# Performance work log

Hardware: AMD Instinct MI355X
Metric: run time of the kernel (lower is better)

The kernel has to match this reference:

```python
import jax, jax.numpy as jnp
import numpy as np

N = 50000
E = 800000
IN_C = 128
HID = 32
HEADS = 8
OUT_C = 64
NEG_SLOPE = 0.2


def setup_inputs() -> dict:
    key = jax.random.key(0)
    ks = jax.random.split(key, 12)
    x = jax.random.normal(ks[0], (N, IN_C), dtype=jnp.float32)
    edge_index = jax.random.randint(ks[1], (2, E), 0, N, dtype=jnp.int64)
    s = 0.05
    W1 = jax.random.normal(ks[2], (IN_C, HEADS * HID), dtype=jnp.float32) * s
    a1_src = jax.random.normal(ks[3], (HEADS, HID), dtype=jnp.float32) * s
    a1_dst = jax.random.normal(ks[4], (HEADS, HID), dtype=jnp.float32) * s
    b1 = jnp.zeros((HEADS * HID,), dtype=jnp.float32)
    W2 = jax.random.normal(ks[5], (HEADS * HID, OUT_C), dtype=jnp.float32) * s
    a2_src = jax.random.normal(ks[6], (1, OUT_C), dtype=jnp.float32) * s
    a2_dst = jax.random.normal(ks[7], (1, OUT_C), dtype=jnp.float32) * s
    b2 = jnp.zeros((OUT_C,), dtype=jnp.float32)
    return {"x": x, "edge_index": edge_index, "W1": W1, "a1_src": a1_src,
            "a1_dst": a1_dst, "b1": b1, "W2": W2, "a2_src": a2_src,
            "a2_dst": a2_dst, "b2": b2}


def gat_conv(x, W, a_src, a_dst, bias, src, dst, concat):
    # x: [N, F_in]; W: [F_in, H*C]; a_src/a_dst: [H, C]
    H, C = a_src.shape
    h = (x @ W).reshape(N, H, C)                      # [N, H, C]
    alpha_s = jnp.einsum('nhc,hc->nh', h, a_src)      # [N, H]
    alpha_d = jnp.einsum('nhc,hc->nh', h, a_dst)
    e = alpha_s[src] + alpha_d[dst]                   # [E, H]
    e = jnp.where(e >= 0, e, NEG_SLOPE * e)           # leaky relu
    # segment softmax over destination nodes
    m = jax.ops.segment_max(e, dst, num_segments=N)   # [N, H]
    e = jnp.exp(e - m[dst])
    z = jax.ops.segment_sum(e, dst, num_segments=N)   # [N, H]
    alpha = e / z[dst]                                # [E, H]
    msg = h[src] * alpha[:, :, None]                  # [E, H, C]
    out = jax.ops.segment_sum(msg, dst, num_segments=N)  # [N, H, C]
    if concat:
        out = out.reshape(N, H * C)
    else:
        out = out.mean(axis=1)
    return out + bias


def reference(x, edge_index, W1, a1_src, a1_dst, b1, W2, a2_src, a2_dst, b2):
    src, dst = edge_index[0], edge_index[1]
    # dropout omitted (eval mode)
    h = gat_conv(x, W1, a1_src, a1_dst, b1, src, dst, concat=True)
    h = jax.nn.elu(h)
    out = gat_conv(h, W2, a2_src, a2_dst, b2, src, dst, concat=False)
    return out
```

## Files before the change

kernel.cpp:

```cpp
#include <hip/hip_runtime.h>
#include <cstdint>
#include <cstddef>

#define N_NODES 50000
#define N_EDGES 800000
#define INC 128
#define HID 32
#define HEADS 8
#define OUTC 64
#define F1 (HEADS * HID)
#define NEG 0.2f
#define CAP 64

typedef unsigned short bf16_t;
typedef __attribute__((ext_vector_type(8))) short bf16x8;
typedef __attribute__((ext_vector_type(4))) float f32x4;

__device__ __forceinline__ float bf2f(bf16_t u) {
  union { unsigned int i; float f; } v;
  v.i = ((unsigned int)u) << 16;
  return v.f;
}
__device__ __forceinline__ bf16_t f2bf(float x) {
  union { float f; unsigned int u; } v;
  v.f = x;
  unsigned int r = v.u + 0x7FFFu + ((v.u >> 16) & 1u);
  return (bf16_t)(r >> 16);
}
__device__ __forceinline__ float lrexp(float v) {
  return expf((v >= 0.f) ? v : NEG * v);
}

__global__ __launch_bounds__(256) void prep(
    const float* __restrict__ W1, const float* __restrict__ W2,
    bf16_t* __restrict__ W1T, bf16_t* __restrict__ W2T, int* __restrict__ cnt) {
  int t = blockIdx.x * 256 + threadIdx.x;
  if (t < N_NODES) cnt[t] = 0;
  if (t < INC * F1) {
    int k = t >> 8, n = t & 255;
    W1T[(size_t)n * INC + k] = f2bf(W1[t]);
  }
  if (t < F1 * OUTC) {
    int k = t >> 6, n = t & 63;
    W2T[(size_t)n * F1 + k] = f2bf(W2[t]);
  }
}

template <bool AF32, int HPT, int HTOT>
__global__ __launch_bounds__(256) void mfma_gemm_fused(
    const void* __restrict__ Av, const bf16_t* __restrict__ Wt,
    bf16_t* __restrict__ C, const float* __restrict__ a_src,
    const float* __restrict__ a_dst, float* __restrict__ as,
    float* __restrict__ ad, int M, int N, int K,
    const int* __restrict__ srcE, const int* __restrict__ dstE,
    int* __restrict__ cnt, int* __restrict__ bucket) {
  constexpr int BM = 64, BN = 64, BK = 64;
  __shared__ union SM {
    bf16_t A[BM * BK];
    struct { float ct[64][65]; float pr[64][4]; } epi;
  } sm;

  const int tid = threadIdx.x;

  if (cnt != nullptr) {
    int eid = (blockIdx.y * gridDim.x + blockIdx.x) * 256 + tid;
    if (eid < N_EDGES) {
      int dd = dstE[eid];
      int pos = atomicAdd(&cnt[dd], 1);
      bucket[(size_t)dd * CAP + pos] = srcE[eid];
    }
  }

  const int wave = tid >> 6, lane = tid & 63;
  const int wm = (wave >> 1) * 32, wn = (wave & 1) * 32;
  const int lr = lane & 15, lq = lane >> 4;
  const int m0 = blockIdx.y * BM, n0 = blockIdx.x * BN;
  const float* A32 = (const float*)Av;
  const bf16_t* A16 = (const bf16_t*)Av;

  f32x4 acc[2][2] = {};

  for (int k0 = 0; k0 < K; k0 += BK) {
    bf16x8 bcur[2][2];
#pragma unroll
    for (int ni = 0; ni < 2; ni++) {
      const size_t brow = (size_t)(n0 + wn + ni * 16 + lr) * K;
#pragma unroll
      for (int kk = 0; kk < 2; kk++)
        bcur[kk][ni] = *reinterpret_cast<const bf16x8*>(
            &Wt[brow + k0 + kk * 32 + lq * 8]);
    }

#pragma unroll
    for (int p = 0; p < 2; p++) {
      int id = p * 256 + tid;
      int r = id >> 3, c = id & 7;
      int gm = m0 + r;
      uint4 v = make_uint4(0, 0, 0, 0);
      if constexpr (AF32) {
        if (gm < M) {
          const float4* ap =
              reinterpret_cast<const float4*>(&A32[(size_t)gm * K + k0 + c * 8]);
          float4 v0 = ap[0], v1 = ap[1];
          union { bf16_t h[8]; uint4 u; } pk;
          pk.h[0] = f2bf(v0.x); pk.h[1] = f2bf(v0.y);
          pk.h[2] = f2bf(v0.z); pk.h[3] = f2bf(v0.w);
          pk.h[4] = f2bf(v1.x); pk.h[5] = f2bf(v1.y);
          pk.h[6] = f2bf(v1.z); pk.h[7] = f2bf(v1.w);
          v = pk.u;
        }
      } else {
        if (gm < M) v = *reinterpret_cast<const uint4*>(&A16[(size_t)gm * K + k0 + c * 8]);
      }
      *reinterpret_cast<uint4*>(&sm.A[r * BK + ((c ^ (r & 7)) * 8)]) = v;
    }
    __syncthreads();
#pragma unroll
    for (int kk = 0; kk < 2; kk++) {
      bf16x8 af[2];
#pragma unroll
      for (int mi = 0; mi < 2; mi++) {
        int rr = wm + mi * 16 + lr;
        af[mi] = *reinterpret_cast<const bf16x8*>(
            &sm.A[rr * BK + (((kk * 4 + lq) ^ (rr & 7)) * 8)]);
      }
#pragma unroll
      for (int mi = 0; mi < 2; mi++)
#pragma unroll
        for (int ni = 0; ni < 2; ni++)
          acc[mi][ni] = __builtin_amdgcn_mfma_f32_16x16x32_bf16(
              af[mi], bcur[kk][ni], acc[mi][ni], 0, 0, 0);
    }
    __syncthreads();
  }

#pragma unroll
  for (int mi = 0; mi < 2; mi++)
#pragma unroll
    for (int ni = 0; ni < 2; ni++)
#pragma unroll
      for (int r = 0; r < 4; r++)
        sm.epi.ct[wm + mi * 16 + lq * 4 + r][wn + ni * 16 + lr] = acc[mi][ni][r];
  __syncthreads();

  {
    int row = tid >> 2, ch = tid & 3;
    int gm = m0 + row;
    if (gm < M) {
      union { bf16_t h[8]; uint4 u; } pk0, pk1;
#pragma unroll
      for (int c = 0; c < 8; c++) pk0.h[c] = f2bf(sm.epi.ct[row][ch * 16 + c]);
#pragma unroll
      for (int c = 0; c < 8; c++) pk1.h[c] = f2bf(sm.epi.ct[row][ch * 16 + 8 + c]);
      *reinterpret_cast<uint4*>(&C[(size_t)gm * N + n0 + ch * 16]) = pk0.u;
      *reinterpret_cast<uint4*>(&C[(size_t)gm * N + n0 + ch * 16 + 8]) = pk1.u;
    }
  }

  {
    int row = tid >> 2, part = tid & 3;
    int gn = m0 + row;
    const float* av = ((part & 2) ? a_dst : a_src) + n0 + (part & 1) * 32;
    float dot = 0.f;
#pragma unroll
    for (int c = 0; c < 32; c++) dot += sm.epi.ct[row][(part & 1) * 32 + c] * av[c];
    if constexpr (HPT == 2) {
      if (gn < M) {
        float* tgt = (part & 2) ? ad : as;
        tgt[(size_t)gn * HTOT + (n0 >> 5) + (part & 1)] = dot;
      }
    } else {
      sm.epi.pr[row][part] = dot;
      __syncthreads();
      if (part == 0 && gn < M) {
        as[gn] = sm.epi.pr[row][0] + sm.epi.pr[row][1];
        ad[gn] = sm.epi.pr[row][2] + sm.epi.pr[row][3];
      }
    }
  }
}

__global__ __launch_bounds__(256) void gat_aggr1(
    const int* __restrict__ cnt, const int* __restrict__ bucket,
    const float* __restrict__ as, const float* __restrict__ ad,
    const bf16_t* __restrict__ hb, const float* __restrict__ bias,
    bf16_t* __restrict__ outp) {
  int d = blockIdx.x * 4 + (threadIdx.x >> 6);
  int lane = threadIdx.x & 63;
  if (d >= N_NODES) return;
  int deg = cnt[d];
  const int* bkt = bucket + (size_t)d * CAP;
  const int sh = lane & 7;
  const int es = lane >> 3;
  const int ah = lane >> 3;
  float ad_h = ad[(size_t)d * 8 + sh];
  float a0 = 0.f, a1 = 0.f, a2 = 0.f, a3 = 0.f, zacc = 0.f;

  if (deg > 0) {
    int ei = es;
    int s_reg = bkt[(ei < deg) ? ei : deg - 1];
    float w_reg = (ei < deg) ? lrexp(as[(size_t)s_reg * 8 + sh] + ad_h) : 0.f;

    for (int cb = 0; cb < deg; cb += 8) {
      const bf16_t* bs[8];
#pragma unroll
      for (int e = 0; e < 8; e++)
        bs[e] = hb + (size_t)__builtin_amdgcn_readlane(s_reg, e << 3) * F1;
      uint2 g[8];
#pragma unroll
      for (int e = 0; e < 8; e++)
        g[e] = *reinterpret_cast<const uint2*>(bs[e] + 4 * lane);
      float w_cur = w_reg;
      zacc += w_reg;
      int nxt = cb + 8;
      if (nxt < deg) {
        int ei2 = nxt + es;
        s_reg = bkt[(ei2 < deg) ? ei2 : deg - 1];
        w_reg = (ei2 < deg) ? lrexp(as[(size_t)s_reg * 8 + sh] + ad_h) : 0.f;
      }
#pragma unroll
      for (int e = 0; e < 8; e++) {
        float wv = __shfl(w_cur, (e << 3) | ah);
        union { uint2 u; bf16_t h[4]; } ld;
        ld.u = g[e];
        a0 += bf2f(ld.h[0]) * wv;
        a1 += bf2f(ld.h[1]) * wv;
        a2 += bf2f(ld.h[2]) * wv;
        a3 += bf2f(ld.h[3]) * wv;
      }
    }
  }

  float zr = zacc;
  zr += __shfl_xor(zr, 8);
  zr += __shfl_xor(zr, 16);
  zr += __shfl_xor(zr, 32);
  float z = __shfl(zr, ah);

  float inv = (deg > 0) ? (1.f / z) : 0.f;
  float4 bv = *reinterpret_cast<const float4*>(&bias[4 * lane]);
  float v0 = a0 * inv + bv.x;
  float v1 = a1 * inv + bv.y;
  float v2 = a2 * inv + bv.z;
  float v3 = a3 * inv + bv.w;
  v0 = (v0 > 0.f) ? v0 : expm1f(v0);
  v1 = (v1 > 0.f) ? v1 : expm1f(v1);
  v2 = (v2 > 0.f) ? v2 : expm1f(v2);
  v3 = (v3 > 0.f) ? v3 : expm1f(v3);
  union { bf16_t h[4]; uint2 u; } pk;
  pk.h[0] = f2bf(v0); pk.h[1] = f2bf(v1); pk.h[2] = f2bf(v2); pk.h[3] = f2bf(v3);
  *reinterpret_cast<uint2*>(&outp[(size_t)d * F1 + 4 * lane]) = pk.u;
}

__global__ __launch_bounds__(256) void gat_aggr2(
    const int* __restrict__ cnt, const int* __restrict__ bucket,
    const float* __restrict__ as, const float* __restrict__ ad,
    const bf16_t* __restrict__ hb, const float* __restrict__ bias,
    float* __restrict__ outp) {
  int d = blockIdx.x * 32 + (threadIdx.x >> 3);
  int sub = threadIdx.x & 7;
  if (d >= N_NODES) return;
  int deg = cnt[d];
  const int* bkt = bucket + (size_t)d * CAP;
  float ad_d = ad[d];
  float acc[8] = {};
  float zacc = 0.f;

  if (deg > 0) {
    int ei = sub;
    int s_reg = bkt[(ei < deg) ? ei : deg - 1];
    float w_reg = (ei < deg) ? lrexp(as[s_reg] + ad_d) : 0.f;

    for (int cb = 0; cb < deg; cb += 8) {
      int sv[8];
#pragma unroll
      for (int e = 0; e < 8; e++) sv[e] = __shfl(s_reg, e, 8);
      uint4 g[8];
#pragma unroll
      for (int e = 0; e < 8; e++)
        g[e] = *reinterpret_cast<const uint4*>(&hb[(size_t)sv[e] * OUTC + 8 * sub]);
      float w_cur = w_reg;
      zacc += w_reg;
      int nxt = cb + 8;
      if (nxt < deg) {
        int ei2 = nxt + sub;
        s_reg = bkt[(ei2 < deg) ? ei2 : deg - 1];
        w_reg = (ei2 < deg) ? lrexp(as[s_reg] + ad_d) : 0.f;
      }
#pragma unroll
      for (int e = 0; e < 8; e++) {
        float wv = __shfl(w_cur, e, 8);
        union { uint4 u; bf16_t h[8]; } ld;
        ld.u = g[e];
#pragma unroll
        for (int q = 0; q < 8; q++) acc[q] += bf2f(ld.h[q]) * wv;
      }
    }
  }

  float zr = zacc;
  zr += __shfl_xor(zr, 1, 8);
  zr += __shfl_xor(zr, 2, 8);
  zr += __shfl_xor(zr, 4, 8);

  float inv = (deg > 0) ? (1.f / zr) : 0.f;
  float4 o0, o1;
  o0.x = acc[0] * inv + bias[8 * sub + 0];
  o0.y = acc[1] * inv + bias[8 * sub + 1];
  o0.z = acc[2] * inv + bias[8 * sub + 2];
  o0.w = acc[3] * inv + bias[8 * sub + 3];
  o1.x = acc[4] * inv + bias[8 * sub + 4];
  o1.y = acc[5] * inv + bias[8 * sub + 5];
  o1.z = acc[6] * inv + bias[8 * sub + 6];
  o1.w = acc[7] * inv + bias[8 * sub + 7];
  *reinterpret_cast<float4*>(&outp[(size_t)d * OUTC + 8 * sub]) = o0;
  *reinterpret_cast<float4*>(&outp[(size_t)d * OUTC + 8 * sub + 4]) = o1;
}

extern "C" void kernel_launch(void* const* d_in, const int* in_sizes, int n_in,
                              void* d_out, int out_size, void* d_ws, size_t ws_size,
                              hipStream_t stream) {
  const float* x      = (const float*)d_in[0];
  const int*   ei     = (const int*)d_in[1];
  const float* W1     = (const float*)d_in[2];
  const float* a1_src = (const float*)d_in[3];
  const float* a1_dst = (const float*)d_in[4];
  const float* b1     = (const float*)d_in[5];
  const float* W2     = (const float*)d_in[6];
  const float* a2_src = (const float*)d_in[7];
  const float* a2_dst = (const float*)d_in[8];
  const float* b2     = (const float*)d_in[9];

  const int* src = ei;
  const int* dst = ei + N_EDGES;
  float* out = (float*)d_out;

  char* base = (char*)d_ws;
  size_t off = 0;
  auto carve = [&](size_t bytes) {
    void* q = base + off;
    off += (bytes + 255) & ~size_t(255);
    return q;
  };
  bf16_t* h1b  = (bf16_t*)carve((size_t)N_NODES * F1 * 2);
  bf16_t* o1b  = (bf16_t*)carve((size_t)N_NODES * F1 * 2);
  bf16_t* h2b  = (bf16_t*)carve((size_t)N_NODES * OUTC * 2);
  float* as1 = (float*)carve((size_t)N_NODES * HEADS * 4);
  float* ad1 = (float*)carve((size_t)N_NODES * HEADS * 4);
  float* as2 = (float*)carve((size_t)N_NODES * 4);
  float* ad2 = (float*)carve((size_t)N_NODES * 4);
  int* cnt = (int*)carve((size_t)N_NODES * 4);
  int* bucket = (int*)carve((size_t)N_NODES * CAP * 4);
  bf16_t* w1t = (bf16_t*)carve((size_t)F1 * INC * 2);
  bf16_t* w2t = (bf16_t*)carve((size_t)OUTC * F1 * 2);

  prep<<<(N_NODES + 255) / 256, 256, 0, stream>>>(W1, W2, w1t, w2t, cnt);

  mfma_gemm_fused<true, 2, HEADS><<<dim3(F1 / 64, (N_NODES + 63) / 64), 256, 0, stream>>>(
      x, w1t, h1b, a1_src, a1_dst, as1, ad1, N_NODES, F1, INC, src, dst, cnt, bucket);

  gat_aggr1<<<(N_NODES + 3) / 4, 256, 0, stream>>>(cnt, bucket, as1, ad1, h1b, b1, o1b);

  mfma_gemm_fused<false, 1, 1><<<dim3(OUTC / 64, (N_NODES + 63) / 64), 256, 0, stream>>>(
      o1b, w2t, h2b, a2_src, a2_dst, as2, ad2, N_NODES, OUTC, F1,
      nullptr, nullptr, nullptr, nullptr);

  gat_aggr2<<<(N_NODES + 31) / 32, 256, 0, stream>>>(cnt, bucket, as2, ad2, h2b, b2, out);
}
```

Baseline: 242.3 us.

## Pre-convert x to bf16, persistent GEMM with double-buffered loads, 16-bit edge buckets

The prep kernel now converts x to bf16, so the first GEMM streams bf16 A instead of converting fp32 inside every column tile. The GEMM becomes a grid-stride persistent kernel (capped at 2048 blocks for layer 1) with a two-stage register prefetch of A and B tiles, and edge bucketing moves into that tile loop. Bucket source indices are stored as 16-bit values, halving bucket traffic, and h2 reuses the h1 buffer. Node indices reach 50000, which fits in unsigned 16 bits, but the prefetch loop assumes K is a multiple of 128 and adds extra barriers.

```diff
diff --git a/kernel.cpp b/kernel.cpp
--- a/kernel.cpp
+++ b/kernel.cpp
@@ -13,6 +13,7 @@
 #define CAP 64
 
 typedef unsigned short bf16_t;
+typedef unsigned short u16;
 typedef __attribute__((ext_vector_type(8))) short bf16x8;
 typedef __attribute__((ext_vector_type(4))) float f32x4;
 
@@ -32,9 +33,20 @@
 }
 
 __global__ __launch_bounds__(256) void prep(
-    const float* __restrict__ W1, const float* __restrict__ W2,
+    const float* __restrict__ x, const float* __restrict__ W1,
+    const float* __restrict__ W2, bf16_t* __restrict__ xb,
     bf16_t* __restrict__ W1T, bf16_t* __restrict__ W2T, int* __restrict__ cnt) {
   int t = blockIdx.x * 256 + threadIdx.x;
+  if (t < (N_NODES * INC) / 8) {
+    const float4* xp = reinterpret_cast<const float4*>(x + (size_t)t * 8);
+    float4 v0 = xp[0], v1 = xp[1];
+    union { bf16_t h[8]; uint4 u; } pk;
+    pk.h[0] = f2bf(v0.x); pk.h[1] = f2bf(v0.y);
+    pk.h[2] = f2bf(v0.z); pk.h[3] = f2bf(v0.w);
+    pk.h[4] = f2bf(v1.x); pk.h[5] = f2bf(v1.y);
+    pk.h[6] = f2bf(v1.z); pk.h[7] = f2bf(v1.w);
+    *reinterpret_cast<uint4*>(xb + (size_t)t * 8) = pk.u;
+  }
   if (t < N_NODES) cnt[t] = 0;
   if (t < INC * F1) {
     int k = t >> 8, n = t & 255;
@@ -46,14 +58,14 @@
   }
 }
 
-template <bool AF32, int HPT, int HTOT>
+template <int HPT, int HTOT>
 __global__ __launch_bounds__(256) void mfma_gemm_fused(
-    const void* __restrict__ Av, const bf16_t* __restrict__ Wt,
+    const bf16_t* __restrict__ A16, const bf16_t* __restrict__ Wt,
     bf16_t* __restrict__ C, const float* __restrict__ a_src,
     const float* __restrict__ a_dst, float* __restrict__ as,
-    float* __restrict__ ad, int M, int N, int K,
+    float* __restrict__ ad, int M, int N, int K, int numTiles,
     const int* __restrict__ srcE, const int* __restrict__ dstE,
-    int* __restrict__ cnt, int* __restrict__ bucket) {
+    int* __restrict__ cnt, u16* __restrict__ bucket) {
   constexpr int BM = 64, BN = 64, BK = 64;
   __shared__ union SM {
     bf16_t A[BM * BK];
@@ -61,127 +73,133 @@
   } sm;
 
   const int tid = threadIdx.x;
-
-  if (cnt != nullptr) {
-    int eid = (blockIdx.y * gridDim.x + blockIdx.x) * 256 + tid;
-    if (eid < N_EDGES) {
-      int dd = dstE[eid];
-      int pos = atomicAdd(&cnt[dd], 1);
-      bucket[(size_t)dd * CAP + pos] = srcE[eid];
-    }
-  }
-
   const int wave = tid >> 6, lane = tid & 63;
   const int wm = (wave >> 1) * 32, wn = (wave & 1) * 32;
   const int lr = lane & 15, lq = lane >> 4;
-  const int m0 = blockIdx.y * BM, n0 = blockIdx.x * BN;
-  const float* A32 = (const float*)Av;
-  const bf16_t* A16 = (const bf16_t*)Av;
-
-  f32x4 acc[2][2] = {};
-
-  for (int k0 = 0; k0 < K; k0 += BK) {
-    bf16x8 bcur[2][2];
-#pragma unroll
-    for (int ni = 0; ni < 2; ni++) {
-      const size_t brow = (size_t)(n0 + wn + ni * 16 + lr) * K;
-#pragma unroll
-      for (int kk = 0; kk < 2; kk++)
-        bcur[kk][ni] = *reinterpret_cast<const bf16x8*>(
-            &Wt[brow + k0 + kk * 32 + lq * 8]);
-    }
-
-#pragma unroll
-    for (int p = 0; p < 2; p++) {
-      int id = p * 256 + tid;
-      int r = id >> 3, c = id & 7;
-      int gm = m0 + r;
-      uint4 v = make_uint4(0, 0, 0, 0);
-      if constexpr (AF32) {
-        if (gm < M) {
-          const float4* ap =
-              reinterpret_cast<const float4*>(&A32[(size_t)gm * K + k0 + c * 8]);
-          float4 v0 = ap[0], v1 = ap[1];
-          union { bf16_t h[8]; uint4 u; } pk;
-          pk.h[0] = f2bf(v0.x); pk.h[1] = f2bf(v0.y);
-          pk.h[2] = f2bf(v0.z); pk.h[3] = f2bf(v0.w);
-          pk.h[4] = f2bf(v1.x); pk.h[5] = f2bf(v1.y);
-          pk.h[6] = f2bf(v1.z); pk.h[7] = f2bf(v1.w);
-          v = pk.u;
+  const int r0 = tid >> 3, c0 = tid & 7;
+  const int r1 = 32 + r0;
+  const int ntx = N >> 6;
+
+  for (int t = blockIdx.x; t < numTiles; t += gridDim.x) {
+    if (cnt != nullptr) {
+      int eid = t * 256 + tid;
+      if (eid < N_EDGES) {
+        int dd = dstE[eid];
+        int pos = atomicAdd(&cnt[dd], 1);
+        bucket[(size_t)dd * CAP + pos] = (u16)srcE[eid];
+      }
+    }
+    const int m0 = (t / ntx) * BM, n0 = (t % ntx) * BN;
+
+    f32x4 acc[2][2] = {};
+
+    auto loadA = [&](int k0, uint4& v0, uint4& v1) {
+      int gm0 = m0 + r0, gm1 = m0 + r1;
+      v0 = (gm0 < M) ? *reinterpret_cast<const uint4*>(&A16[(size_t)gm0 * K + k0 + c0 * 8])
+                     : make_uint4(0, 0, 0, 0);
+      v1 = (gm1 < M) ? *reinterpret_cast<const uint4*>(&A16[(size_t)gm1 * K + k0 + c0 * 8])
+                     : make_uint4(0, 0, 0, 0);
+    };
+    auto writeA = [&](const uint4& v0, const uint4& v1) {
+      *reinterpret_cast<uint4*>(&sm.A[r0 * BK + ((c0 ^ (r0 & 7)) * 8)]) = v0;
+      *reinterpret_cast<uint4*>(&sm.A[r1 * BK + ((c0 ^ (r1 & 7)) * 8)]) = v1;
+    };
+    auto loadB = [&](int k0, bf16x8 (&b)[2][2]) {
+#pragma unroll
+      for (int ni = 0; ni < 2; ni++) {
+        const size_t brow = (size_t)(n0 + wn + ni * 16 + lr) * K;
+#pragma unroll
+        for (int kk = 0; kk < 2; kk++)
+          b[kk][ni] = *reinterpret_cast<const bf16x8*>(&Wt[brow + k0 + kk * 32 + lq * 8]);
+      }
+    };
+    auto mstep = [&](const bf16x8 (&b)[2][2]) {
+#pragma unroll
+      for (int kk = 0; kk < 2; kk++) {
+        bf16x8 af[2];
+#pragma unroll
+        for (int mi = 0; mi < 2; mi++) {
+          int rr = wm + mi * 16 + lr;
+          af[mi] = *reinterpret_cast<const bf16x8*>(
+              &sm.A[rr * BK + (((kk * 4 + lq) ^ (rr & 7)) * 8)]);
+        }
+#pragma unroll
+        for (int mi = 0; mi < 2; mi++)
+#pragma unroll
+          for (int ni = 0; ni < 2; ni++)
+            acc[mi][ni] = __builtin_amdgcn_mfma_f32_16x16x32_bf16(
+                af[mi], b[kk][ni], acc[mi][ni], 0, 0, 0);
+      }
+    };
+
+    uint4 pa0, pa1, qa0, qa1;
+    bf16x8 b0[2][2], b1[2][2];
+    loadA(0, pa0, pa1);
+    for (int k0 = 0; k0 < K; k0 += 2 * BK) {
+      loadB(k0, b0);
+      writeA(pa0, pa1);
+      loadA(k0 + BK, qa0, qa1);
+      loadB(k0 + BK, b1);
+      __syncthreads();
+      mstep(b0);
+      __syncthreads();
+      writeA(qa0, qa1);
+      if (k0 + 2 * BK < K) loadA(k0 + 2 * BK, pa0, pa1);
+      __syncthreads();
+      mstep(b1);
+      __syncthreads();
+    }
+
+#pragma unroll
+    for (int mi = 0; mi < 2; mi++)
+#pragma unroll
+      for (int ni = 0; ni < 2; ni++)
+#pragma unroll
+        for (int r = 0; r < 4; r++)
+          sm.epi.ct[wm + mi * 16 + lq * 4 + r][wn + ni * 16 + lr] = acc[mi][ni][r];
+    __syncthreads();
+
+    {
+      int row = tid >> 2, ch = tid & 3;
+      int gm = m0 + row;
+      if (gm < M) {
+        union { bf16_t h[8]; uint4 u; } pk0, pk1;
+#pragma unroll
+        for (int c = 0; c < 8; c++) pk0.h[c] = f2bf(sm.epi.ct[row][ch * 16 + c]);
+#pragma unroll
+        for (int c = 0; c < 8; c++) pk1.h[c] = f2bf(sm.epi.ct[row][ch * 16 + 8 + c]);
+        *reinterpret_cast<uint4*>(&C[(size_t)gm * N + n0 + ch * 16]) = pk0.u;
+        *reinterpret_cast<uint4*>(&C[(size_t)gm * N + n0 + ch * 16 + 8]) = pk1.u;
+      }
+    }
+
+    {
+      int row = tid >> 2, part = tid & 3;
+      int gn = m0 + row;
+      const float* av = ((part & 2) ? a_dst : a_src) + n0 + (part & 1) * 32;
+      float dot = 0.f;
+#pragma unroll
+      for (int c = 0; c < 32; c++) dot += sm.epi.ct[row][(part & 1) * 32 + c] * av[c];
+      if constexpr (HPT == 2) {
+        if (gn < M) {
+          float* tgt = (part & 2) ? ad : as;
+          tgt[(size_t)gn * HTOT + (n0 >> 5) + (part & 1)] = dot;
         }
       } else {
-        if (gm < M) v = *reinterpret_cast<const uint4*>(&A16[(size_t)gm * K + k0 + c * 8]);
-      }
-      *reinterpret_cast<uint4*>(&sm.A[r * BK + ((c ^ (r & 7)) * 8)]) = v;
+        sm.epi.pr[row][part] = dot;
+        __syncthreads();
+        if (part == 0 && gn < M) {
+          as[gn] = sm.epi.pr[row][0] + sm.epi.pr[row][1];
+          ad[gn] = sm.epi.pr[row][2] + sm.epi.pr[row][3];
+        }
+      }
     }
     __syncthreads();
-#pragma unroll
-    for (int kk = 0; kk < 2; kk++) {
-      bf16x8 af[2];
-#pragma unroll
-      for (int mi = 0; mi < 2; mi++) {
-        int rr = wm + mi * 16 + lr;
-        af[mi] = *reinterpret_cast<const bf16x8*>(
-            &sm.A[rr * BK + (((kk * 4 + lq) ^ (rr & 7)) * 8)]);
-      }
-#pragma unroll
-      for (int mi = 0; mi < 2; mi++)
-#pragma unroll
-        for (int ni = 0; ni < 2; ni++)
-          acc[mi][ni] = __builtin_amdgcn_mfma_f32_16x16x32_bf16(
-              af[mi], bcur[kk][ni], acc[mi][ni], 0, 0, 0);
-    }
-    __syncthreads();
-  }
-
-#pragma unroll
-  for (int mi = 0; mi < 2; mi++)
-#pragma unroll
-    for (int ni = 0; ni < 2; ni++)
-#pragma unroll
-      for (int r = 0; r < 4; r++)
-        sm.epi.ct[wm + mi * 16 + lq * 4 + r][wn + ni * 16 + lr] = acc[mi][ni][r];
-  __syncthreads();
-
-  {
-    int row = tid >> 2, ch = tid & 3;
-    int gm = m0 + row;
-    if (gm < M) {
-      union { bf16_t h[8]; uint4 u; } pk0, pk1;
-#pragma unroll
-      for (int c = 0; c < 8; c++) pk0.h[c] = f2bf(sm.epi.ct[row][ch * 16 + c]);
-#pragma unroll
-      for (int c = 0; c < 8; c++) pk1.h[c] = f2bf(sm.epi.ct[row][ch * 16 + 8 + c]);
-      *reinterpret_cast<uint4*>(&C[(size_t)gm * N + n0 + ch * 16]) = pk0.u;
-      *reinterpret_cast<uint4*>(&C[(size_t)gm * N + n0 + ch * 16 + 8]) = pk1.u;
-    }
-  }
-
-  {
-    int row = tid >> 2, part = tid & 3;
-    int gn = m0 + row;
-    const float* av = ((part & 2) ? a_dst : a_src) + n0 + (part & 1) * 32;
-    float dot = 0.f;
-#pragma unroll
-    for (int c = 0; c < 32; c++) dot += sm.epi.ct[row][(part & 1) * 32 + c] * av[c];
-    if constexpr (HPT == 2) {
-      if (gn < M) {
-        float* tgt = (part & 2) ? ad : as;
-        tgt[(size_t)gn * HTOT + (n0 >> 5) + (part & 1)] = dot;
-      }
-    } else {
-      sm.epi.pr[row][part] = dot;
-      __syncthreads();
-      if (part == 0 && gn < M) {
-        as[gn] = sm.epi.pr[row][0] + sm.epi.pr[row][1];
-        ad[gn] = sm.epi.pr[row][2] + sm.epi.pr[row][3];
-      }
-    }
   }
 }
 
 __global__ __launch_bounds__(256) void gat_aggr1(
-    const int* __restrict__ cnt, const int* __restrict__ bucket,
+    const int* __restrict__ cnt, const u16* __restrict__ bucket,
     const float* __restrict__ as, const float* __restrict__ ad,
     const bf16_t* __restrict__ hb, const float* __restrict__ bias,
     bf16_t* __restrict__ outp) {
@@ -189,7 +207,7 @@
   int lane = threadIdx.x & 63;
   if (d >= N_NODES) return;
   int deg = cnt[d];
-  const int* bkt = bucket + (size_t)d * CAP;
+  const u16* bkt = bucket + (size_t)d * CAP;
   const int sh = lane & 7;
   const int es = lane >> 3;
   const int ah = lane >> 3;
@@ -198,7 +216,7 @@
 
   if (deg > 0) {
     int ei = es;
-    int s_reg = bkt[(ei < deg) ? ei : deg - 1];
+    int s_reg = (int)bkt[(ei < deg) ? ei : deg - 1];
     float w_reg = (ei < deg) ? lrexp(as[(size_t)s_reg * 8 + sh] + ad_h) : 0.f;
 
     for (int cb = 0; cb < deg; cb += 8) {
@@ -215,7 +233,7 @@
       int nxt = cb + 8;
       if (nxt < deg) {
         int ei2 = nxt + es;
-        s_reg = bkt[(ei2 < deg) ? ei2 : deg - 1];
+        s_reg = (int)bkt[(ei2 < deg) ? ei2 : deg - 1];
         w_reg = (ei2 < deg) ? lrexp(as[(size_t)s_reg * 8 + sh] + ad_h) : 0.f;
       }
 #pragma unroll
@@ -253,7 +271,7 @@
 }
 
 __global__ __launch_bounds__(256) void gat_aggr2(
-    const int* __restrict__ cnt, const int* __restrict__ bucket,
+    const int* __restrict__ cnt, const u16* __restrict__ bucket,
     const float* __restrict__ as, const float* __restrict__ ad,
     const bf16_t* __restrict__ hb, const float* __restrict__ bias,
     float* __restrict__ outp) {
@@ -261,14 +279,14 @@
   int sub = threadIdx.x & 7;
   if (d >= N_NODES) return;
   int deg = cnt[d];
-  const int* bkt = bucket + (size_t)d * CAP;
+  const u16* bkt = bucket + (size_t)d * CAP;
   float ad_d = ad[d];
   float acc[8] = {};
   float zacc = 0.f;
 
   if (deg > 0) {
     int ei = sub;
-    int s_reg = bkt[(ei < deg) ? ei : deg - 1];
+    int s_reg = (int)bkt[(ei < deg) ? ei : deg - 1];
     float w_reg = (ei < deg) ? lrexp(as[s_reg] + ad_d) : 0.f;
 
     for (int cb = 0; cb < deg; cb += 8) {
@@ -284,7 +302,7 @@
       int nxt = cb + 8;
       if (nxt < deg) {
         int ei2 = nxt + sub;
-        s_reg = bkt[(ei2 < deg) ? ei2 : deg - 1];
+        s_reg = (int)bkt[(ei2 < deg) ? ei2 : deg - 1];
         w_reg = (ei2 < deg) ? lrexp(as[s_reg] + ad_d) : 0.f;
       }
 #pragma unroll
@@ -344,26 +362,36 @@
   };
   bf16_t* h1b  = (bf16_t*)carve((size_t)N_NODES * F1 * 2);
   bf16_t* o1b  = (bf16_t*)carve((size_t)N_NODES * F1 * 2);
-  bf16_t* h2b  = (bf16_t*)carve((size_t)N_NODES * OUTC * 2);
   float* as1 = (float*)carve((size_t)N_NODES * HEADS * 4);
   float* ad1 = (float*)carve((size_t)N_NODES * HEADS * 4);
   float* as2 = (float*)carve((size_t)N_NODES * 4);
   float* ad2 = (float*)carve((size_t)N_NODES * 4);
   int* cnt = (int*)carve((size_t)N_NODES * 4);
-  int* bucket = (int*)carve((size_t)N_NODES * CAP * 4);
+  u16* bucket = (u16*)carve((size_t)N_NODES * CAP * 2);
   bf16_t* w1t = (bf16_t*)carve((size_t)F1 * INC * 2);
   bf16_t* w2t = (bf16_t*)carve((size_t)OUTC * F1 * 2);
-
-  prep<<<(N_NODES + 255) / 256, 256, 0, stream>>>(W1, W2, w1t, w2t, cnt);
-
-  mfma_gemm_fused<true, 2, HEADS><<<dim3(F1 / 64, (N_NODES + 63) / 64), 256, 0, stream>>>(
-      x, w1t, h1b, a1_src, a1_dst, as1, ad1, N_NODES, F1, INC, src, dst, cnt, bucket);
+  bf16_t* xb  = (bf16_t*)carve((size_t)N_NODES * INC * 2);
+  bf16_t* h2b = h1b;
+
+  prep<<<(N_NODES * INC / 8 + 255) / 256, 256, 0, stream>>>(
+      x, W1, W2, xb, w1t, w2t, cnt);
+
+  {
+    int numTiles = ((N_NODES + 63) / 64) * (F1 / 64);
+    int grid = numTiles < 2048 ? numTiles : 2048;
+    mfma_gemm_fused<2, HEADS><<<grid, 256, 0, stream>>>(
+        xb, w1t, h1b, a1_src, a1_dst, as1, ad1, N_NODES, F1, INC, numTiles,
+        src, dst, cnt, bucket);
+  }
 
   gat_aggr1<<<(N_NODES + 3) / 4, 256, 0, stream>>>(cnt, bucket, as1, ad1, h1b, b1, o1b);
 
-  mfma_gemm_fused<false, 1, 1><<<dim3(OUTC / 64, (N_NODES + 63) / 64), 256, 0, stream>>>(
-      o1b, w2t, h2b, a2_src, a2_dst, as2, ad2, N_NODES, OUTC, F1,
-      nullptr, nullptr, nullptr, nullptr);
+  {
+    int numTiles = ((N_NODES + 63) / 64) * (OUTC / 64);
+    mfma_gemm_fused<1, 1><<<numTiles, 256, 0, stream>>>(
+        o1b, w2t, h2b, a2_src, a2_dst, as2, ad2, N_NODES, OUTC, F1, numTiles,
+        nullptr, nullptr, nullptr, nullptr);
+  }
 
   gat_aggr2<<<(N_NODES + 31) / 32, 256, 0, stream>>>(cnt, bucket, as2, ad2, h2b, b2, out);
 }
```

Result: no change. 240.7 us (-0.7%).
